# Optimization experiments

Measured on AMD Instinct MI355X. Metric: run time of the kernel, lower is better.

Reference implementation:

```python
import jax, jax.numpy as jnp
import numpy as np

B, N, D = 32, 64, 256

def _gelu(x):
    return jax.nn.gelu(x, approximate=False)

def setup_inputs() -> dict:
    key = jax.random.key(0)
    ks = jax.random.split(key, 16)
    def w(k, shape):
        fan_in = shape[0]
        return (jax.random.normal(k, shape, jnp.float32) / np.float32(np.sqrt(fan_in)))
    return {
        "dataset_embedding": jax.random.normal(ks[0], (B, D), jnp.float32),
        "variable_embeddings": jax.random.normal(ks[1], (B, N, D), jnp.float32),
        "claim_context": jax.random.normal(ks[2], (B, D), jnp.float32),
        "dge_w1": w(ks[3], (2 * D, D)), "dge_b1": jnp.zeros((D,), jnp.float32),
        "dge_w2": w(ks[4], (D, D)),     "dge_b2": jnp.zeros((D,), jnp.float32),
        "cge_w1": w(ks[5], (2 * D, D)), "cge_b1": jnp.zeros((D,), jnp.float32),
        "cge_w2": w(ks[6], (D, D)),     "cge_b2": jnp.zeros((D,), jnp.float32),
        "dep_w1": w(ks[7], (4 * D, D)), "dep_b1": jnp.zeros((D,), jnp.float32),
        "dep_w2": w(ks[8], (D, 1)),     "dep_b2": jnp.zeros((1,), jnp.float32),
        "cep_w1": w(ks[9], (4 * D, D)), "cep_b1": jnp.zeros((D,), jnp.float32),
        "cep_w2": w(ks[10], (D, 1)),    "cep_b2": jnp.zeros((1,), jnp.float32),
        "gate_w1": w(ks[11], (3, 64)),  "gate_b1": jnp.zeros((64,), jnp.float32),
        "gate_w2": w(ks[12], (64, 1)),  "gate_b2": jnp.zeros((1,), jnp.float32),
        "n_samples": 500,
    }

def _encode(ve, ctx, w1, b1, w2, b2):
    # Sequential(Linear(2d,d), GELU, Linear(d,d), GELU); dropout=0 (eval)
    x = jnp.concatenate([ve, jnp.broadcast_to(ctx[:, None, :], ve.shape)], axis=-1)
    h = _gelu(x @ w1 + b1)
    return _gelu(h @ w2 + b2)

def _predict_edges(ve_enc, ctx, w1, b1, w2, b2):
    # var_with_context: [B,N,2D]; edge features cat([var_i, var_j]) @ w1
    # == (vwc @ w1[:2D]) broadcast over i + (vwc @ w1[2D:]) broadcast over j
    vwc = jnp.concatenate([ve_enc, jnp.broadcast_to(ctx[:, None, :], ve_enc.shape)], axis=-1)
    wi, wj = w1[: 2 * D], w1[2 * D :]
    fi = vwc @ wi  # [B,N,D]
    fj = vwc @ wj  # [B,N,D]
    h = _gelu(fi[:, :, None, :] + fj[:, None, :, :] + b1)  # [B,N,N,D]
    logits = jnp.einsum("bijd,do->bij", h, w2) + b2[0]
    eye = jnp.eye(N, dtype=bool)
    return jnp.where(eye[None, :, :], jnp.float32(-1e9), logits)

def reference(dataset_embedding, variable_embeddings, claim_context,
              dge_w1, dge_b1, dge_w2, dge_b2,
              cge_w1, cge_b1, cge_w2, cge_b2,
              dep_w1, dep_b1, dep_w2, dep_b2,
              cep_w1, cep_b1, cep_w2, cep_b2,
              gate_w1, gate_b1, gate_w2, gate_b2,
              n_samples):
    avg_claim_confidence = 0.5
    var_data = _encode(variable_embeddings, dataset_embedding, dge_w1, dge_b1, dge_w2, dge_b2)
    var_claim = _encode(variable_embeddings, claim_context, cge_w1, cge_b1, cge_w2, cge_b2)
    W_data_logits = _predict_edges(var_data, dataset_embedding, dep_w1, dep_b1, dep_w2, dep_b2)
    W_claim_logits = _predict_edges(var_claim, claim_context, cep_w1, cep_b1, cep_w2, cep_b2)

    p = jax.nn.sigmoid(W_data_logits)
    eps = jnp.float32(1e-8)
    data_entropy = -(p * jnp.log(p + eps) + (1 - p) * jnp.log(1 - p + eps)).mean(axis=(1, 2))  # [B]

    ns = jnp.full((B,), min(n_samples / 1000.0, 1.0), jnp.float32)
    cc = jnp.full((B,), avg_claim_confidence, jnp.float32)
    gf = jnp.stack([ns, cc, data_entropy], axis=-1)  # [B,3]
    gate = jax.nn.sigmoid(_gelu(gf @ gate_w1 + gate_b1) @ gate_w2 + gate_b2)  # [B,1]
    gate = gate[:, :, None]  # [B,1,1]

    W_post_logits = gate * W_data_logits + (1 - gate) * W_claim_logits

    # NOTEARS: h(W) = tr(expm(W o W)) - n, W = sigmoid(logits)
    Wsig = jax.nn.sigmoid(W_post_logits)
    M = jax.vmap(jax.scipy.linalg.expm)(Wsig * Wsig)
    acyc = (jnp.trace(M, axis1=1, axis2=2) - N).mean()

    W_posterior = jax.nn.sigmoid(W_post_logits)
    return (W_posterior, acyc)
```

## Files before the change

### kernel.cpp

```cpp
#include <hip/hip_runtime.h>
#include <hip/hip_bf16.h>


#define LDS_STRIDE 260
#define ES 68

__device__ __forceinline__ float gelu_f(float x) {
    float z = fabsf(x) * 0.70710678118654752440f;
    float t = __builtin_amdgcn_rcpf(fmaf(0.3275911f, z, 1.0f));
    float p = t * fmaf(t, fmaf(t, fmaf(t, fmaf(t, 1.061405429f, -1.453152027f),
                                       1.421413741f), -0.284496736f), 0.254829592f);
    float e = __expf(-z * z);
    float erfv = fmaf(-p, e, 1.0f);
    erfv = copysignf(erfv, x);
    return 0.5f * x * (1.0f + erfv);
}
__device__ __forceinline__ float sigmoid_f(float x) {
    return 1.0f / (1.0f + expf(-x));
}
__device__ __forceinline__ float f4c(const float4& v, int k) {
    return k == 0 ? v.x : k == 1 ? v.y : k == 2 ? v.z : v.w;
}
__device__ __forceinline__ float4 ld4(const float* __restrict__ buf, int r, int c) {
    return *(const float4*)&buf[r * ES + c];
}

__global__ __launch_bounds__(256) void k0_ctx(
    const float* __restrict__ ds, const float* __restrict__ cc,
    const float* __restrict__ dge_w1, const float* __restrict__ dge_b1,
    const float* __restrict__ cge_w1, const float* __restrict__ cge_b1,
    const float* __restrict__ dep_w1, const float* __restrict__ dep_b1,
    const float* __restrict__ cep_w1, const float* __restrict__ cep_b1,
    float* __restrict__ ctxproj)
{
    const int b = blockIdx.x;
    const int which = blockIdx.y;
    const float* ctx; const float* W; const float* bias;
    switch (which) {
        case 0:  ctx = ds; W = dge_w1 + 256 * 256; bias = dge_b1; break;
        case 1:  ctx = cc; W = cge_w1 + 256 * 256; bias = cge_b1; break;
        case 2:  ctx = ds; W = dep_w1 + 256 * 256; bias = dep_b1; break;
        case 3:  ctx = ds; W = dep_w1 + 768 * 256; bias = nullptr; break;
        case 4:  ctx = cc; W = cep_w1 + 256 * 256; bias = cep_b1; break;
        default: ctx = cc; W = cep_w1 + 768 * 256; bias = nullptr; break;
    }
    __shared__ float sctx[256];
    const int tid = threadIdx.x;
    sctx[tid] = ctx[b * 256 + tid];
    __syncthreads();
    float acc = 0.0f;
    #pragma unroll 2
    for (int k = 0; k < 256; k += 4) {
        float4 c4 = *(const float4*)&sctx[k];
        acc = fmaf(c4.x, W[(k + 0) * 256 + tid], acc);
        acc = fmaf(c4.y, W[(k + 1) * 256 + tid], acc);
        acc = fmaf(c4.z, W[(k + 2) * 256 + tid], acc);
        acc = fmaf(c4.w, W[(k + 3) * 256 + tid], acc);
    }
    if (bias) acc += bias[tid];
    ctxproj[(which * 32 + b) * 256 + tid] = acc;
}

__device__ __forceinline__ void gemm_ks(const float* __restrict__ src,
                                        const float* __restrict__ W,
                                        int ks0, int t0, float acc[8][4])
{
    #pragma unroll
    for (int r = 0; r < 8; ++r)
        #pragma unroll
        for (int c = 0; c < 4; ++c) acc[r][c] = 0.0f;
    #pragma unroll 2
    for (int k = ks0; k < ks0 + 32; k += 4) {
        float4 wv0 = *(const float4*)&W[(k + 0) * 256 + t0];
        float4 wv1 = *(const float4*)&W[(k + 1) * 256 + t0];
        float4 wv2 = *(const float4*)&W[(k + 2) * 256 + t0];
        float4 wv3 = *(const float4*)&W[(k + 3) * 256 + t0];
        float4 a[8];
        #pragma unroll
        for (int r = 0; r < 8; ++r) a[r] = *(const float4*)&src[r * LDS_STRIDE + k];
        float4 wvs[4] = {wv0, wv1, wv2, wv3};
        #pragma unroll
        for (int kk = 0; kk < 4; ++kk) {
            float4 wv = wvs[kk];
            #pragma unroll
            for (int r = 0; r < 8; ++r) {
                float av = f4c(a[r], kk);
                acc[r][0] = fmaf(av, wv.x, acc[r][0]);
                acc[r][1] = fmaf(av, wv.y, acc[r][1]);
                acc[r][2] = fmaf(av, wv.z, acc[r][2]);
                acc[r][3] = fmaf(av, wv.w, acc[r][3]);
            }
        }
    }
}

__device__ __forceinline__ void write_part(float* __restrict__ part, int w, int t0,
                                           const float acc[8][4])
{
    #pragma unroll
    for (int r = 0; r < 8; ++r) {
        float4 o = {acc[r][0], acc[r][1], acc[r][2], acc[r][3]};
        *(float4*)&part[(w * 8 + r) * 256 + t0] = o;
    }
}

__device__ __forceinline__ float4 reduce_part(const float* __restrict__ part, int r, int t0)
{
    float4 s = {0.0f, 0.0f, 0.0f, 0.0f};
    #pragma unroll
    for (int w = 0; w < 8; ++w) {
        float4 v = *(const float4*)&part[(w * 8 + r) * 256 + t0];
        s.x += v.x; s.y += v.y; s.z += v.z; s.w += v.w;
    }
    return s;
}

__global__ __launch_bounds__(512) void k1_encode(
    const float* __restrict__ ve_g,
    const float* __restrict__ dge_w1, const float* __restrict__ dge_w2, const float* __restrict__ dge_b2,
    const float* __restrict__ cge_w1, const float* __restrict__ cge_w2, const float* __restrict__ cge_b2,
    const float* __restrict__ dep_w1, const float* __restrict__ cep_w1,
    const float* __restrict__ ctxproj,
    float* __restrict__ fi_dep, float* __restrict__ fjt_dep,
    float* __restrict__ fi_cep, float* __restrict__ fjt_cep)
{
    __shared__ float sve[8 * LDS_STRIDE];
    __shared__ float sA[8 * LDS_STRIDE];
    __shared__ float sB[8 * LDS_STRIDE];
    __shared__ float part[8 * 8 * 256];

    const int tid = threadIdx.x;
    const int b = blockIdx.x >> 3;
    const int chunk = blockIdx.x & 7;
    const int n0 = chunk * 8;

    const int w  = tid >> 6;
    const int t0 = (tid & 63) * 4;
    const int ks0 = w * 32;

    {
        int idx = tid * 4;
        int r = idx >> 8, k = idx & 255;
        *(float4*)&sve[r * LDS_STRIDE + k] = *(const float4*)&ve_g[(b * 64 + n0) * 256 + idx];
    }
    __syncthreads();

    float acc[8][4];

    gemm_ks(sve, dge_w1, ks0, t0, acc);
    write_part(part, w, t0, acc);
    __syncthreads();
    {
        float4 s = reduce_part(part, w, t0);
        float4 cp = *(const float4*)&ctxproj[(0 * 32 + b) * 256 + t0];
        float4 o = {gelu_f(s.x + cp.x), gelu_f(s.y + cp.y), gelu_f(s.z + cp.z), gelu_f(s.w + cp.w)};
        *(float4*)&sA[w * LDS_STRIDE + t0] = o;
    }
    __syncthreads();

    gemm_ks(sA, dge_w2, ks0, t0, acc);
    write_part(part, w, t0, acc);
    __syncthreads();
    {
        float4 s = reduce_part(part, w, t0);
        float4 bv = *(const float4*)&dge_b2[t0];
        float4 o = {gelu_f(s.x + bv.x), gelu_f(s.y + bv.y), gelu_f(s.z + bv.z), gelu_f(s.w + bv.w)};
        *(float4*)&sB[w * LDS_STRIDE + t0] = o;
    }
    __syncthreads();

    gemm_ks(sB, dep_w1, ks0, t0, acc);
    write_part(part, w, t0, acc);
    __syncthreads();
    {
        float4 s = reduce_part(part, w, t0);
        float4 cp = *(const float4*)&ctxproj[(2 * 32 + b) * 256 + t0];
        float4 o = {s.x + cp.x, s.y + cp.y, s.z + cp.z, s.w + cp.w};
        *(float4*)&fi_dep[(b * 64 + n0 + w) * 256 + t0] = o;
    }
    __syncthreads();

    gemm_ks(sB, dep_w1 + 512 * 256, ks0, t0, acc);
    write_part(part, w, t0, acc);
    __syncthreads();
    {
        float4 s = reduce_part(part, w, t0);
        float4 cp = *(const float4*)&ctxproj[(3 * 32 + b) * 256 + t0];
        float4 o = {s.x + cp.x, s.y + cp.y, s.z + cp.z, s.w + cp.w};
        *(float4*)&sA[w * LDS_STRIDE + t0] = o;
    }
    __syncthreads();
    {
        int t = tid & 255, half = tid >> 8;
        float v0 = sA[(half * 4 + 0) * LDS_STRIDE + t];
        float v1 = sA[(half * 4 + 1) * LDS_STRIDE + t];
        float v2 = sA[(half * 4 + 2) * LDS_STRIDE + t];
        float v3 = sA[(half * 4 + 3) * LDS_STRIDE + t];
        float4 o = {v0, v1, v2, v3};
        *(float4*)&fjt_dep[(b * 256 + t) * 64 + n0 + half * 4] = o;
    }

    gemm_ks(sve, cge_w1, ks0, t0, acc);
    write_part(part, w, t0, acc);
    __syncthreads();
    {
        float4 s = reduce_part(part, w, t0);
        float4 cp = *(const float4*)&ctxproj[(1 * 32 + b) * 256 + t0];
        float4 o = {gelu_f(s.x + cp.x), gelu_f(s.y + cp.y), gelu_f(s.z + cp.z), gelu_f(s.w + cp.w)};
        *(float4*)&sB[w * LDS_STRIDE + t0] = o;
    }
    __syncthreads();

    gemm_ks(sB, cge_w2, ks0, t0, acc);
    write_part(part, w, t0, acc);
    __syncthreads();
    {
        float4 s = reduce_part(part, w, t0);
        float4 bv = *(const float4*)&cge_b2[t0];
        float4 o = {gelu_f(s.x + bv.x), gelu_f(s.y + bv.y), gelu_f(s.z + bv.z), gelu_f(s.w + bv.w)};
        *(float4*)&sA[w * LDS_STRIDE + t0] = o;
    }
    __syncthreads();

    gemm_ks(sA, cep_w1, ks0, t0, acc);
    write_part(part, w, t0, acc);
    __syncthreads();
    {
        float4 s = reduce_part(part, w, t0);
        float4 cp = *(const float4*)&ctxproj[(4 * 32 + b) * 256 + t0];
        float4 o = {s.x + cp.x, s.y + cp.y, s.z + cp.z, s.w + cp.w};
        *(float4*)&fi_cep[(b * 64 + n0 + w) * 256 + t0] = o;
    }
    __syncthreads();

    gemm_ks(sA, cep_w1 + 512 * 256, ks0, t0, acc);
    write_part(part, w, t0, acc);
    __syncthreads();
    {
        float4 s = reduce_part(part, w, t0);
        float4 cp = *(const float4*)&ctxproj[(5 * 32 + b) * 256 + t0];
        float4 o = {s.x + cp.x, s.y + cp.y, s.z + cp.z, s.w + cp.w};
        *(float4*)&sB[w * LDS_STRIDE + t0] = o;
    }
    __syncthreads();
    {
        int t = tid & 255, half = tid >> 8;
        float v0 = sB[(half * 4 + 0) * LDS_STRIDE + t];
        float v1 = sB[(half * 4 + 1) * LDS_STRIDE + t];
        float v2 = sB[(half * 4 + 2) * LDS_STRIDE + t];
        float v3 = sB[(half * 4 + 3) * LDS_STRIDE + t];
        float4 o = {v0, v1, v2, v3};
        *(float4*)&fjt_cep[(b * 256 + t) * 64 + n0 + half * 4] = o;
    }
}

__global__ __launch_bounds__(512) void k3_edges(
    const float* __restrict__ fi_dep, const float* __restrict__ fjt_dep,
    const float* __restrict__ fi_cep, const float* __restrict__ fjt_cep,
    const float* __restrict__ dep_w2, const float* __restrict__ dep_b2,
    const float* __restrict__ cep_w2, const float* __restrict__ cep_b2,
    float* __restrict__ Wd, float* __restrict__ Wc, float* __restrict__ entp)
{
    __shared__ float fjD_s[64 * 64];
    __shared__ float fjC_s[64 * 64];
    __shared__ float fiD_s[4][256];
    __shared__ float fiC_s[4][256];
    __shared__ float w2D_s[256];
    __shared__ float w2C_s[256];
    __shared__ float redD[8][64];
    __shared__ float redC[8][64];

    const int b   = blockIdx.x >> 4;
    const int ig  = blockIdx.x & 15;
    const int tid = threadIdx.x;
    const int s   = tid >> 6;
    const int j   = tid & 63;
    const int row = s & 3;
    const int dh  = s >> 2;

    if (tid < 256) {
        int rr = tid >> 6, c = (tid & 63) * 4;
        *(float4*)&fiD_s[rr][c] = *(const float4*)&fi_dep[(b * 64 + ig * 4 + rr) * 256 + c];
    } else {
        int t2 = tid - 256;
        int rr = t2 >> 6, c = (t2 & 63) * 4;
        *(float4*)&fiC_s[rr][c] = *(const float4*)&fi_cep[(b * 64 + ig * 4 + rr) * 256 + c];
    }
    if (tid < 64) {
        *(float4*)&w2D_s[tid * 4] = *(const float4*)&dep_w2[tid * 4];
    } else if (tid < 128) {
        int t = tid - 64;
        *(float4*)&w2C_s[t * 4] = *(const float4*)&cep_w2[t * 4];
    }

    float accD = 0.0f, accC = 0.0f;

    for (int c0 = 0; c0 < 256; c0 += 64) {
        if (c0) __syncthreads();
        {
            const float4* sD = (const float4*)(fjt_dep + (b * 256 + c0) * 64);
            const float4* sC = (const float4*)(fjt_cep + (b * 256 + c0) * 64);
            ((float4*)fjD_s)[tid]       = sD[tid];
            ((float4*)fjD_s)[tid + 512] = sD[tid + 512];
            ((float4*)fjC_s)[tid]       = sC[tid];
            ((float4*)fjC_s)[tid + 512] = sC[tid + 512];
        }
        __syncthreads();

        const int d0 = dh * 32;
        #pragma unroll 4
        for (int d = d0; d < d0 + 32; d += 2) {
            float fid0 = fiD_s[row][c0 + d];
            float fid1 = fiD_s[row][c0 + d + 1];
            float fic0 = fiC_s[row][c0 + d];
            float fic1 = fiC_s[row][c0 + d + 1];
            float fjd0 = fjD_s[(d + 0) * 64 + j];
            float fjd1 = fjD_s[(d + 1) * 64 + j];
            float fjc0 = fjC_s[(d + 0) * 64 + j];
            float fjc1 = fjC_s[(d + 1) * 64 + j];
            float wd0 = w2D_s[c0 + d], wd1 = w2D_s[c0 + d + 1];
            float wc0 = w2C_s[c0 + d], wc1 = w2C_s[c0 + d + 1];
            accD = fmaf(gelu_f(fid0 + fjd0), wd0, accD);
            accD = fmaf(gelu_f(fid1 + fjd1), wd1, accD);
            accC = fmaf(gelu_f(fic0 + fjc0), wc0, accC);
            accC = fmaf(gelu_f(fic1 + fjc1), wc1, accC);
        }
    }

    redD[s][j] = accD;
    redC[s][j] = accC;
    __syncthreads();

    if (s < 4) {
        const int i = ig * 4 + s;
        float lD = (redD[s][j] + redD[s + 4][j]) + dep_b2[0];
        float lC = (redC[s][j] + redC[s + 4][j]) + cep_b2[0];
        if (j == i) { lD = -1e9f; lC = -1e9f; }
        Wd[(b * 64 + i) * 64 + j] = lD;
        Wc[(b * 64 + i) * 64 + j] = lC;

        float p = sigmoid_f(lD);
        float e = -(p * logf(p + 1e-8f) + (1.0f - p) * logf(1.0f - p + 1e-8f));
        #pragma unroll
        for (int off = 32; off; off >>= 1) e += __shfl_down(e, off);
        if (j == 0) entp[b * 64 + i] = e;
    }
}

__device__ __forceinline__ void mm64f(const float* __restrict__ A, const float* __restrict__ B,
                                      int r0, int c0, float acc[4][4])
{
    #pragma unroll
    for (int i = 0; i < 4; ++i)
        #pragma unroll
        for (int j = 0; j < 4; ++j) acc[i][j] = 0.0f;
    for (int kb = 0; kb < 64; kb += 4) {
        float4 xa[4];
        #pragma unroll
        for (int i = 0; i < 4; ++i) xa[i] = ld4(A, r0 + i, kb);
        #pragma unroll
        for (int kk = 0; kk < 4; ++kk) {
            float4 rv = ld4(B, kb + kk, c0);
            float rj[4] = {rv.x, rv.y, rv.z, rv.w};
            #pragma unroll
            for (int i = 0; i < 4; ++i) {
                float xv = f4c(xa[i], kk);
                #pragma unroll
                for (int j = 0; j < 4; ++j) acc[i][j] = fmaf(xv, rj[j], acc[i][j]);
            }
        }
    }
}

__device__ __forceinline__ void mm64d(const float* __restrict__ A, const float* __restrict__ B,
                                      int r0, int c0, double acc[4][4])
{
    #pragma unroll
    for (int i = 0; i < 4; ++i)
        #pragma unroll
        for (int j = 0; j < 4; ++j) acc[i][j] = 0.0;
    for (int kb = 0; kb < 64; kb += 4) {
        float4 xa[4];
        #pragma unroll
        for (int i = 0; i < 4; ++i) xa[i] = ld4(A, r0 + i, kb);
        #pragma unroll
        for (int kk = 0; kk < 4; ++kk) {
            float4 rv = ld4(B, kb + kk, c0);
            double rj[4] = {(double)rv.x, (double)rv.y, (double)rv.z, (double)rv.w};
            #pragma unroll
            for (int i = 0; i < 4; ++i) {
                double xv = (double)f4c(xa[i], kk);
                #pragma unroll
                for (int j = 0; j < 4; ++j) acc[i][j] = fma(xv, rj[j], acc[i][j]);
            }
        }
    }
}

__global__ __launch_bounds__(256) void k6_gate_expm(
    const float* __restrict__ Wd, const float* __restrict__ Wc,
    const float* __restrict__ entp,
    const float* __restrict__ gw1, const float* __restrict__ gb1,
    const float* __restrict__ gw2, const float* __restrict__ gb2,
    const int* __restrict__ n_samples,
    float* __restrict__ out, float* __restrict__ traces)
{
    __shared__ float Xs [64 * ES];
    __shared__ float X2s[64 * ES];
    __shared__ float X3s[64 * ES];
    __shared__ float Ra [64 * ES];
    __shared__ float Rb [64 * ES];
    __shared__ float sgate;
    __shared__ float sent;
    __shared__ int ssexp;

    const int b = blockIdx.x;
    const int tid = threadIdx.x;

    const float C2 = 0.5f, C3 = 1.0f/6.0f, C4 = 1.0f/24.0f, C5 = 1.0f/120.0f;
    const float C6 = 1.0f/720.0f, C7 = 1.0f/5040.0f, C8 = 1.0f/40320.0f;
    const float C9 = 1.0f/362880.0f, C10 = 1.0f/3628800.0f, C11 = 1.0f/39916800.0f;
    const float C12 = 1.0f/479001600.0f, C13 = 1.0f/6227020800.0f;

    if (tid == 0) {
        float s = 0.0f;
        for (int c = 0; c < 64; ++c) s += entp[b * 64 + c];
        sent = s / 4096.0f;
    }
    __syncthreads();
    if (tid < 64) {
        float ns = fminf((float)n_samples[0] / 1000.0f, 1.0f);
        float ccf = 0.5f;
        float pre = ns * gw1[tid] + ccf * gw1[64 + tid] + sent * gw1[128 + tid] + gb1[tid];
        float hid = gelu_f(pre) * gw2[tid];
        #pragma unroll
        for (int off = 32; off; off >>= 1) hid += __shfl_down(hid, off);
        if (tid == 0) sgate = sigmoid_f(hid + gb2[0]);
    }
    __syncthreads();
    const float g = sgate;

    for (int idx = tid; idx < 4096; idx += 256) {
        float d = Wd[b * 4096 + idx];
        float c = Wc[b * 4096 + idx];
        float post = g * d + (1.0f - g) * c;
        float sg = sigmoid_f(post);
        out[b * 4096 + idx] = sg;
        Xs[(idx >> 6) * ES + (idx & 63)] = sg * sg;
    }
    __syncthreads();

    if (tid < 64) {
        float cs = 0.0f;
        for (int r = 0; r < 64; ++r) cs += Xs[r * ES + tid];
        #pragma unroll
        for (int off = 32; off; off >>= 1) cs = fmaxf(cs, __shfl_down(cs, off));
        if (tid == 0) {
            int se = 0;
            if (cs > 1.0f) se = (int)ceilf(log2f(cs));
            if (se < 0) se = 0;
            if (se > 12) se = 12;
            ssexp = se;
        }
    }
    __syncthreads();
    const int sexp = ssexp;
    const float scale = ldexpf(1.0f, -sexp);
    for (int idx = tid; idx < 4096; idx += 256) {
        Xs[(idx >> 6) * ES + (idx & 63)] *= scale;
    }
    __syncthreads();

    const int rq = tid >> 4, cq = tid & 15;
    const int r0 = rq * 4, c0 = cq * 4;
    float acc[4][4];

    mm64f(Xs, Xs, r0, c0, acc);
    #pragma unroll
    for (int i = 0; i < 4; ++i) {
        float4 o = {acc[i][0], acc[i][1], acc[i][2], acc[i][3]};
        *(float4*)&X2s[(r0 + i) * ES + c0] = o;
    }
    __syncthreads();

    mm64f(X2s, Xs, r0, c0, acc);
    #pragma unroll
    for (int i = 0; i < 4; ++i) {
        float4 o = {acc[i][0], acc[i][1], acc[i][2], acc[i][3]};
        *(float4*)&X3s[(r0 + i) * ES + c0] = o;
    }
    __syncthreads();

    mm64f(Xs, X3s, r0, c0, acc);
    #pragma unroll
    for (int i = 0; i < 4; ++i) {
        float4 xv = ld4(Xs, r0 + i, c0);
        float4 x2 = ld4(X2s, r0 + i, c0);
        float4 x3 = ld4(X3s, r0 + i, c0);
        float o[4];
        #pragma unroll
        for (int j = 0; j < 4; ++j) {
            o[j] = C13 * acc[i][j] + C12 * f4c(x3, j) + C10 * f4c(xv, j) + C11 * f4c(x2, j)
                 + ((r0 + i) == (c0 + j) ? C9 : 0.0f);
        }
        float4 ov = {o[0], o[1], o[2], o[3]};
        *(float4*)&Ra[(r0 + i) * ES + c0] = ov;
    }
    __syncthreads();

    mm64f(Ra, X3s, r0, c0, acc);
    #pragma unroll
    for (int i = 0; i < 4; ++i) {
        float4 xv = ld4(Xs, r0 + i, c0);
        float4 x2 = ld4(X2s, r0 + i, c0);
        float o[4];
        #pragma unroll
        for (int j = 0; j < 4; ++j) {
            o[j] = acc[i][j] + C7 * f4c(xv, j) + C8 * f4c(x2, j)
                 + ((r0 + i) == (c0 + j) ? C6 : 0.0f);
        }
        float4 ov = {o[0], o[1], o[2], o[3]};
        *(float4*)&Rb[(r0 + i) * ES + c0] = ov;
    }
    __syncthreads();

    mm64f(Rb, X3s, r0, c0, acc);
    #pragma unroll
    for (int i = 0; i < 4; ++i) {
        float4 xv = ld4(Xs, r0 + i, c0);
        float4 x2 = ld4(X2s, r0 + i, c0);
        float o[4];
        #pragma unroll
        for (int j = 0; j < 4; ++j) {
            o[j] = acc[i][j] + C4 * f4c(xv, j) + C5 * f4c(x2, j)
                 + ((r0 + i) == (c0 + j) ? C3 : 0.0f);
        }
        float4 ov = {o[0], o[1], o[2], o[3]};
        *(float4*)&Ra[(r0 + i) * ES + c0] = ov;
    }
    __syncthreads();

    mm64f(Ra, X3s, r0, c0, acc);
    #pragma unroll
    for (int i = 0; i < 4; ++i) {
        float4 xv = ld4(Xs, r0 + i, c0);
        float4 x2 = ld4(X2s, r0 + i, c0);
        float o[4];
        #pragma unroll
        for (int j = 0; j < 4; ++j) {
            o[j] = acc[i][j] + f4c(xv, j) + C2 * f4c(x2, j)
                 + ((r0 + i) == (c0 + j) ? 1.0f : 0.0f);
        }
        float4 ov = {o[0], o[1], o[2], o[3]};
        *(float4*)&Rb[(r0 + i) * ES + c0] = ov;
    }
    __syncthreads();

    float* cur = Rb;
    float* oth = Ra;
    for (int sq = 0; sq < sexp; ++sq) {
        double dacc[4][4];
        mm64d(cur, cur, r0, c0, dacc);
        #pragma unroll
        for (int i = 0; i < 4; ++i) {
            float4 o = {(float)dacc[i][0], (float)dacc[i][1], (float)dacc[i][2], (float)dacc[i][3]};
            *(float4*)&oth[(r0 + i) * ES + c0] = o;
        }
        __syncthreads();
        float* t = cur; cur = oth; oth = t;
    }

    if (tid == 0) {
        double tr = 0.0;
        for (int i = 0; i < 64; ++i) tr += (double)cur[i * ES + i];
        traces[b] = (float)tr;
    }
}

__global__ void k7_acyc(const float* __restrict__ traces, float* __restrict__ out)
{
    if (threadIdx.x == 0 && blockIdx.x == 0) {
        double s = 0.0;
        for (int b = 0; b < 32; ++b) s += (double)traces[b];
        out[131072] = (float)(s / 32.0 - 64.0);
    }
}

extern "C" void kernel_launch(void* const* d_in, const int* in_sizes, int n_in,
                              void* d_out, int out_size, void* d_ws, size_t ws_size,
                              hipStream_t stream)
{
    (void)in_sizes; (void)n_in; (void)out_size; (void)ws_size;

    const float* ds     = (const float*)d_in[0];
    const float* ve     = (const float*)d_in[1];
    const float* cc     = (const float*)d_in[2];
    const float* dge_w1 = (const float*)d_in[3];
    const float* dge_b1 = (const float*)d_in[4];
    const float* dge_w2 = (const float*)d_in[5];
    const float* dge_b2 = (const float*)d_in[6];
    const float* cge_w1 = (const float*)d_in[7];
    const float* cge_b1 = (const float*)d_in[8];
    const float* cge_w2 = (const float*)d_in[9];
    const float* cge_b2 = (const float*)d_in[10];
    const float* dep_w1 = (const float*)d_in[11];
    const float* dep_b1 = (const float*)d_in[12];
    const float* dep_w2 = (const float*)d_in[13];
    const float* dep_b2 = (const float*)d_in[14];
    const float* cep_w1 = (const float*)d_in[15];
    const float* cep_b1 = (const float*)d_in[16];
    const float* cep_w2 = (const float*)d_in[17];
    const float* cep_b2 = (const float*)d_in[18];
    const float* gw1    = (const float*)d_in[19];
    const float* gb1    = (const float*)d_in[20];
    const float* gw2    = (const float*)d_in[21];
    const float* gb2    = (const float*)d_in[22];
    const int*   nsamp  = (const int*)d_in[23];

    float* ws = (float*)d_ws;
    float* ctxproj = ws;
    float* fi_dep  = ctxproj + 49152;
    float* fjt_dep = fi_dep + 524288;
    float* fi_cep  = fjt_dep + 524288;
    float* fjt_cep = fi_cep + 524288;
    float* Wd      = fjt_cep + 524288;
    float* Wc      = Wd + 131072;
    float* entp    = Wc + 131072;
    float* traces  = entp + 2048;

    float* outp = (float*)d_out;

    k0_ctx<<<dim3(32, 6), 256, 0, stream>>>(ds, cc, dge_w1, dge_b1, cge_w1, cge_b1,
                                            dep_w1, dep_b1, cep_w1, cep_b1, ctxproj);
    k1_encode<<<256, 512, 0, stream>>>(ve, dge_w1, dge_w2, dge_b2,
                                       cge_w1, cge_w2, cge_b2,
                                       dep_w1, cep_w1, ctxproj,
                                       fi_dep, fjt_dep, fi_cep, fjt_cep);
    k3_edges<<<512, 512, 0, stream>>>(fi_dep, fjt_dep, fi_cep, fjt_cep,
                                      dep_w2, dep_b2, cep_w2, cep_b2,
                                      Wd, Wc, entp);
    k6_gate_expm<<<32, 256, 0, stream>>>(Wd, Wc, entp, gw1, gb1, gw2, gb2,
                                         nsamp, outp, traces);
    k7_acyc<<<1, 64, 0, stream>>>(traces, outp);
}
```

Measured before the change: 129.5 us.

## Split encoder chains across blocks, halve partial buffer, widen expm kernel

The encoder kernel now runs the data and claim chains in separate blocks (512 blocks instead of 256), which doubles parallelism. The per-block split-K partial buffer is halved by having the upper warps add their partials in place, and context projections are loaded once up front. The expm kernel goes from 256 to 512 threads with 2x4 output tiles, and its scalar loops for the entropy sum and trace become wave shuffle reductions. The scaling threshold also changes so one fewer squaring step is used, which may shift accuracy a little in exchange for less work.

```diff
diff --git a/kernel.cpp b/kernel.cpp
--- a/kernel.cpp
+++ b/kernel.cpp
@@ -94,28 +94,40 @@
     }
 }
 
-__device__ __forceinline__ void write_part(float* __restrict__ part, int w, int t0,
-                                           const float acc[8][4])
-{
-    #pragma unroll
-    for (int r = 0; r < 8; ++r) {
-        float4 o = {acc[r][0], acc[r][1], acc[r][2], acc[r][3]};
-        *(float4*)&part[(w * 8 + r) * 256 + t0] = o;
-    }
-}
-
-__device__ __forceinline__ float4 reduce_part(const float* __restrict__ part, int r, int t0)
+__device__ __forceinline__ void part_write_rmw(float* __restrict__ part, int w, int t0,
+                                               const float acc[8][4])
+{
+    if (w < 4) {
+        #pragma unroll
+        for (int r = 0; r < 8; ++r) {
+            float4 o = {acc[r][0], acc[r][1], acc[r][2], acc[r][3]};
+            *(float4*)&part[(w * 8 + r) * 256 + t0] = o;
+        }
+    }
+    __syncthreads();
+    if (w >= 4) {
+        #pragma unroll
+        for (int r = 0; r < 8; ++r) {
+            float4 v = *(const float4*)&part[((w - 4) * 8 + r) * 256 + t0];
+            float4 o = {v.x + acc[r][0], v.y + acc[r][1], v.z + acc[r][2], v.w + acc[r][3]};
+            *(float4*)&part[((w - 4) * 8 + r) * 256 + t0] = o;
+        }
+    }
+    __syncthreads();
+}
+
+__device__ __forceinline__ float4 reduce4(const float* __restrict__ part, int r, int t0)
 {
     float4 s = {0.0f, 0.0f, 0.0f, 0.0f};
     #pragma unroll
-    for (int w = 0; w < 8; ++w) {
-        float4 v = *(const float4*)&part[(w * 8 + r) * 256 + t0];
+    for (int sl = 0; sl < 4; ++sl) {
+        float4 v = *(const float4*)&part[(sl * 8 + r) * 256 + t0];
         s.x += v.x; s.y += v.y; s.z += v.z; s.w += v.w;
     }
     return s;
 }
 
-__global__ __launch_bounds__(512) void k1_encode(
+__global__ __launch_bounds__(512, 4) void k1_encode(
     const float* __restrict__ ve_g,
     const float* __restrict__ dge_w1, const float* __restrict__ dge_w2, const float* __restrict__ dge_b2,
     const float* __restrict__ cge_w1, const float* __restrict__ cge_w2, const float* __restrict__ cge_b2,
@@ -127,16 +139,33 @@
     __shared__ float sve[8 * LDS_STRIDE];
     __shared__ float sA[8 * LDS_STRIDE];
     __shared__ float sB[8 * LDS_STRIDE];
-    __shared__ float part[8 * 8 * 256];
-
-    const int tid = threadIdx.x;
-    const int b = blockIdx.x >> 3;
-    const int chunk = blockIdx.x & 7;
-    const int n0 = chunk * 8;
+    __shared__ float part[4 * 8 * 256];
+
+    const int tid   = threadIdx.x;
+    const int blk   = blockIdx.x;
+    const int chain = blk & 1;
+    const int chunk = (blk >> 1) & 7;
+    const int b     = blk >> 4;
+    const int n0    = chunk * 8;
+
+    const float* w1   = chain ? cge_w1 : dge_w1;
+    const float* w2   = chain ? cge_w2 : dge_w2;
+    const float* b2   = chain ? cge_b2 : dge_b2;
+    const float* epw  = chain ? cep_w1 : dep_w1;
+    float* fi  = chain ? fi_cep  : fi_dep;
+    float* fjt = chain ? fjt_cep : fjt_dep;
+    const int cp_s1 = chain ? 1 : 0;
+    const int cp_fi = chain ? 4 : 2;
+    const int cp_fj = chain ? 5 : 3;
 
     const int w  = tid >> 6;
     const int t0 = (tid & 63) * 4;
     const int ks0 = w * 32;
+
+    float4 cp1 = *(const float4*)&ctxproj[(cp_s1 * 32 + b) * 256 + t0];
+    float4 bv2 = *(const float4*)&b2[t0];
+    float4 cpf = *(const float4*)&ctxproj[(cp_fi * 32 + b) * 256 + t0];
+    float4 cpj = *(const float4*)&ctxproj[(cp_fj * 32 + b) * 256 + t0];
 
     {
         int idx = tid * 4;
@@ -147,46 +176,40 @@
 
     float acc[8][4];
 
-    gemm_ks(sve, dge_w1, ks0, t0, acc);
-    write_part(part, w, t0, acc);
-    __syncthreads();
+    gemm_ks(sve, w1, ks0, t0, acc);
+    part_write_rmw(part, w, t0, acc);
     {
-        float4 s = reduce_part(part, w, t0);
-        float4 cp = *(const float4*)&ctxproj[(0 * 32 + b) * 256 + t0];
-        float4 o = {gelu_f(s.x + cp.x), gelu_f(s.y + cp.y), gelu_f(s.z + cp.z), gelu_f(s.w + cp.w)};
+        float4 s = reduce4(part, w, t0);
+        float4 o = {gelu_f(s.x + cp1.x), gelu_f(s.y + cp1.y),
+                    gelu_f(s.z + cp1.z), gelu_f(s.w + cp1.w)};
         *(float4*)&sA[w * LDS_STRIDE + t0] = o;
     }
     __syncthreads();
 
-    gemm_ks(sA, dge_w2, ks0, t0, acc);
-    write_part(part, w, t0, acc);
-    __syncthreads();
+    gemm_ks(sA, w2, ks0, t0, acc);
+    part_write_rmw(part, w, t0, acc);
     {
-        float4 s = reduce_part(part, w, t0);
-        float4 bv = *(const float4*)&dge_b2[t0];
-        float4 o = {gelu_f(s.x + bv.x), gelu_f(s.y + bv.y), gelu_f(s.z + bv.z), gelu_f(s.w + bv.w)};
+        float4 s = reduce4(part, w, t0);
+        float4 o = {gelu_f(s.x + bv2.x), gelu_f(s.y + bv2.y),
+                    gelu_f(s.z + bv2.z), gelu_f(s.w + bv2.w)};
         *(float4*)&sB[w * LDS_STRIDE + t0] = o;
     }
     __syncthreads();
 
-    gemm_ks(sB, dep_w1, ks0, t0, acc);
-    write_part(part, w, t0, acc);
-    __syncthreads();
+    gemm_ks(sB, epw, ks0, t0, acc);
+    part_write_rmw(part, w, t0, acc);
     {
-        float4 s = reduce_part(part, w, t0);
-        float4 cp = *(const float4*)&ctxproj[(2 * 32 + b) * 256 + t0];
-        float4 o = {s.x + cp.x, s.y + cp.y, s.z + cp.z, s.w + cp.w};
-        *(float4*)&fi_dep[(b * 64 + n0 + w) * 256 + t0] = o;
-    }
-    __syncthreads();
-
-    gemm_ks(sB, dep_w1 + 512 * 256, ks0, t0, acc);
-    write_part(part, w, t0, acc);
-    __syncthreads();
+        float4 s = reduce4(part, w, t0);
+        float4 o = {s.x + cpf.x, s.y + cpf.y, s.z + cpf.z, s.w + cpf.w};
+        *(float4*)&fi[(b * 64 + n0 + w) * 256 + t0] = o;
+    }
+    __syncthreads();
+
+    gemm_ks(sB, epw + 512 * 256, ks0, t0, acc);
+    part_write_rmw(part, w, t0, acc);
     {
-        float4 s = reduce_part(part, w, t0);
-        float4 cp = *(const float4*)&ctxproj[(3 * 32 + b) * 256 + t0];
-        float4 o = {s.x + cp.x, s.y + cp.y, s.z + cp.z, s.w + cp.w};
+        float4 s = reduce4(part, w, t0);
+        float4 o = {s.x + cpj.x, s.y + cpj.y, s.z + cpj.z, s.w + cpj.w};
         *(float4*)&sA[w * LDS_STRIDE + t0] = o;
     }
     __syncthreads();
@@ -197,60 +220,7 @@
         float v2 = sA[(half * 4 + 2) * LDS_STRIDE + t];
         float v3 = sA[(half * 4 + 3) * LDS_STRIDE + t];
         float4 o = {v0, v1, v2, v3};
-        *(float4*)&fjt_dep[(b * 256 + t) * 64 + n0 + half * 4] = o;
-    }
-
-    gemm_ks(sve, cge_w1, ks0, t0, acc);
-    write_part(part, w, t0, acc);
-    __syncthreads();
-    {
-        float4 s = reduce_part(part, w, t0);
-        float4 cp = *(const float4*)&ctxproj[(1 * 32 + b) * 256 + t0];
-        float4 o = {gelu_f(s.x + cp.x), gelu_f(s.y + cp.y), gelu_f(s.z + cp.z), gelu_f(s.w + cp.w)};
-        *(float4*)&sB[w * LDS_STRIDE + t0] = o;
-    }
-    __syncthreads();
-
-    gemm_ks(sB, cge_w2, ks0, t0, acc);
-    write_part(part, w, t0, acc);
-    __syncthreads();
-    {
-        float4 s = reduce_part(part, w, t0);
-        float4 bv = *(const float4*)&cge_b2[t0];
-        float4 o = {gelu_f(s.x + bv.x), gelu_f(s.y + bv.y), gelu_f(s.z + bv.z), gelu_f(s.w + bv.w)};
-        *(float4*)&sA[w * LDS_STRIDE + t0] = o;
-    }
-    __syncthreads();
-
-    gemm_ks(sA, cep_w1, ks0, t0, acc);
-    write_part(part, w, t0, acc);
-    __syncthreads();
-    {
-        float4 s = reduce_part(part, w, t0);
-        float4 cp = *(const float4*)&ctxproj[(4 * 32 + b) * 256 + t0];
-        float4 o = {s.x + cp.x, s.y + cp.y, s.z + cp.z, s.w + cp.w};
-        *(float4*)&fi_cep[(b * 64 + n0 + w) * 256 + t0] = o;
-    }
-    __syncthreads();
-
-    gemm_ks(sA, cep_w1 + 512 * 256, ks0, t0, acc);
-    write_part(part, w, t0, acc);
-    __syncthreads();
-    {
-        float4 s = reduce_part(part, w, t0);
-        float4 cp = *(const float4*)&ctxproj[(5 * 32 + b) * 256 + t0];
-        float4 o = {s.x + cp.x, s.y + cp.y, s.z + cp.z, s.w + cp.w};
-        *(float4*)&sB[w * LDS_STRIDE + t0] = o;
-    }
-    __syncthreads();
-    {
-        int t = tid & 255, half = tid >> 8;
-        float v0 = sB[(half * 4 + 0) * LDS_STRIDE + t];
-        float v1 = sB[(half * 4 + 1) * LDS_STRIDE + t];
-        float v2 = sB[(half * 4 + 2) * LDS_STRIDE + t];
-        float v3 = sB[(half * 4 + 3) * LDS_STRIDE + t];
-        float4 o = {v0, v1, v2, v3};
-        *(float4*)&fjt_cep[(b * 256 + t) * 64 + n0 + half * 4] = o;
+        *(float4*)&fjt[(b * 256 + t) * 64 + n0 + half * 4] = o;
     }
 }
 
@@ -347,57 +317,57 @@
     }
 }
 
-__device__ __forceinline__ void mm64f(const float* __restrict__ A, const float* __restrict__ B,
-                                      int r0, int c0, float acc[4][4])
-{
-    #pragma unroll
-    for (int i = 0; i < 4; ++i)
+__device__ __forceinline__ void mm64f2(const float* __restrict__ A, const float* __restrict__ B,
+                                       int r0, int c0, float acc[2][4])
+{
+    #pragma unroll
+    for (int i = 0; i < 2; ++i)
         #pragma unroll
         for (int j = 0; j < 4; ++j) acc[i][j] = 0.0f;
     for (int kb = 0; kb < 64; kb += 4) {
-        float4 xa[4];
-        #pragma unroll
-        for (int i = 0; i < 4; ++i) xa[i] = ld4(A, r0 + i, kb);
+        float4 a0 = ld4(A, r0 + 0, kb);
+        float4 a1 = ld4(A, r0 + 1, kb);
         #pragma unroll
         for (int kk = 0; kk < 4; ++kk) {
             float4 rv = ld4(B, kb + kk, c0);
-            float rj[4] = {rv.x, rv.y, rv.z, rv.w};
-            #pragma unroll
-            for (int i = 0; i < 4; ++i) {
-                float xv = f4c(xa[i], kk);
-                #pragma unroll
-                for (int j = 0; j < 4; ++j) acc[i][j] = fmaf(xv, rj[j], acc[i][j]);
-            }
-        }
-    }
-}
-
-__device__ __forceinline__ void mm64d(const float* __restrict__ A, const float* __restrict__ B,
-                                      int r0, int c0, double acc[4][4])
-{
-    #pragma unroll
-    for (int i = 0; i < 4; ++i)
+            float x0 = f4c(a0, kk), x1 = f4c(a1, kk);
+            acc[0][0] = fmaf(x0, rv.x, acc[0][0]);
+            acc[0][1] = fmaf(x0, rv.y, acc[0][1]);
+            acc[0][2] = fmaf(x0, rv.z, acc[0][2]);
+            acc[0][3] = fmaf(x0, rv.w, acc[0][3]);
+            acc[1][0] = fmaf(x1, rv.x, acc[1][0]);
+            acc[1][1] = fmaf(x1, rv.y, acc[1][1]);
+            acc[1][2] = fmaf(x1, rv.z, acc[1][2]);
+            acc[1][3] = fmaf(x1, rv.w, acc[1][3]);
+        }
+    }
+}
+
+__device__ __forceinline__ void mm64d2(const float* __restrict__ A, const float* __restrict__ B,
+                                       int r0, int c0, double acc[2][4])
+{
+    #pragma unroll
+    for (int i = 0; i < 2; ++i)
         #pragma unroll
         for (int j = 0; j < 4; ++j) acc[i][j] = 0.0;
     for (int kb = 0; kb < 64; kb += 4) {
-        float4 xa[4];
-        #pragma unroll
-        for (int i = 0; i < 4; ++i) xa[i] = ld4(A, r0 + i, kb);
+        float4 a0 = ld4(A, r0 + 0, kb);
+        float4 a1 = ld4(A, r0 + 1, kb);
         #pragma unroll
         for (int kk = 0; kk < 4; ++kk) {
             float4 rv = ld4(B, kb + kk, c0);
             double rj[4] = {(double)rv.x, (double)rv.y, (double)rv.z, (double)rv.w};
+            double x0 = (double)f4c(a0, kk), x1 = (double)f4c(a1, kk);
             #pragma unroll
-            for (int i = 0; i < 4; ++i) {
-                double xv = (double)f4c(xa[i], kk);
-                #pragma unroll
-                for (int j = 0; j < 4; ++j) acc[i][j] = fma(xv, rj[j], acc[i][j]);
+            for (int j = 0; j < 4; ++j) {
+                acc[0][j] = fma(x0, rj[j], acc[0][j]);
+                acc[1][j] = fma(x1, rj[j], acc[1][j]);
             }
         }
     }
 }
 
-__global__ __launch_bounds__(256) void k6_gate_expm(
+__global__ __launch_bounds__(512) void k6_gate_expm(
     const float* __restrict__ Wd, const float* __restrict__ Wc,
     const float* __restrict__ entp,
     const float* __restrict__ gw1, const float* __restrict__ gb1,
@@ -422,10 +392,11 @@
     const float C9 = 1.0f/362880.0f, C10 = 1.0f/3628800.0f, C11 = 1.0f/39916800.0f;
     const float C12 = 1.0f/479001600.0f, C13 = 1.0f/6227020800.0f;
 
-    if (tid == 0) {
-        float s = 0.0f;
-        for (int c = 0; c < 64; ++c) s += entp[b * 64 + c];
-        sent = s / 4096.0f;
+    if (tid < 64) {
+        float v = entp[b * 64 + tid];
+        #pragma unroll
+        for (int off = 32; off; off >>= 1) v += __shfl_down(v, off);
+        if (tid == 0) sent = v / 4096.0f;
     }
     __syncthreads();
     if (tid < 64) {
@@ -440,7 +411,7 @@
     __syncthreads();
     const float g = sgate;
 
-    for (int idx = tid; idx < 4096; idx += 256) {
+    for (int idx = tid; idx < 4096; idx += 512) {
         float d = Wd[b * 4096 + idx];
         float c = Wc[b * 4096 + idx];
         float post = g * d + (1.0f - g) * c;
@@ -457,7 +428,7 @@
         for (int off = 32; off; off >>= 1) cs = fmaxf(cs, __shfl_down(cs, off));
         if (tid == 0) {
             int se = 0;
-            if (cs > 1.0f) se = (int)ceilf(log2f(cs));
+            if (cs > 2.0f) se = (int)ceilf(log2f(cs * 0.5f));
             if (se < 0) se = 0;
             if (se > 12) se = 12;
             ssexp = se;
@@ -466,34 +437,34 @@
     __syncthreads();
     const int sexp = ssexp;
     const float scale = ldexpf(1.0f, -sexp);
-    for (int idx = tid; idx < 4096; idx += 256) {
+    for (int idx = tid; idx < 4096; idx += 512) {
         Xs[(idx >> 6) * ES + (idx & 63)] *= scale;
     }
     __syncthreads();
 
-    const int rq = tid >> 4, cq = tid & 15;
-    const int r0 = rq * 4, c0 = cq * 4;
-    float acc[4][4];
-
-    mm64f(Xs, Xs, r0, c0, acc);
-    #pragma unroll
-    for (int i = 0; i < 4; ++i) {
+    const int r0 = (tid >> 4) * 2;
+    const int c0 = (tid & 15) * 4;
+    float acc[2][4];
+
+    mm64f2(Xs, Xs, r0, c0, acc);
+    #pragma unroll
+    for (int i = 0; i < 2; ++i) {
         float4 o = {acc[i][0], acc[i][1], acc[i][2], acc[i][3]};
         *(float4*)&X2s[(r0 + i) * ES + c0] = o;
     }
     __syncthreads();
 
-    mm64f(X2s, Xs, r0, c0, acc);
-    #pragma unroll
-    for (int i = 0; i < 4; ++i) {
+    mm64f2(X2s, Xs, r0, c0, acc);
+    #pragma unroll
+    for (int i = 0; i < 2; ++i) {
         float4 o = {acc[i][0], acc[i][1], acc[i][2], acc[i][3]};
         *(float4*)&X3s[(r0 + i) * ES + c0] = o;
     }
     __syncthreads();
 
-    mm64f(Xs, X3s, r0, c0, acc);
-    #pragma unroll
-    for (int i = 0; i < 4; ++i) {
+    mm64f2(Xs, X3s, r0, c0, acc);
+    #pragma unroll
+    for (int i = 0; i < 2; ++i) {
         float4 xv = ld4(Xs, r0 + i, c0);
         float4 x2 = ld4(X2s, r0 + i, c0);
         float4 x3 = ld4(X3s, r0 + i, c0);
@@ -508,9 +479,9 @@
     }
     __syncthreads();
 
-    mm64f(Ra, X3s, r0, c0, acc);
-    #pragma unroll
-    for (int i = 0; i < 4; ++i) {
+    mm64f2(Ra, X3s, r0, c0, acc);
+    #pragma unroll
+    for (int i = 0; i < 2; ++i) {
         float4 xv = ld4(Xs, r0 + i, c0);
         float4 x2 = ld4(X2s, r0 + i, c0);
         float o[4];
@@ -524,9 +495,9 @@
     }
     __syncthreads();
 
-    mm64f(Rb, X3s, r0, c0, acc);
-    #pragma unroll
-    for (int i = 0; i < 4; ++i) {
+    mm64f2(Rb, X3s, r0, c0, acc);
+    #pragma unroll
+    for (int i = 0; i < 2; ++i) {
         float4 xv = ld4(Xs, r0 + i, c0);
         float4 x2 = ld4(X2s, r0 + i, c0);
         float o[4];
@@ -540,9 +511,9 @@
     }
     __syncthreads();
 
-    mm64f(Ra, X3s, r0, c0, acc);
-    #pragma unroll
-    for (int i = 0; i < 4; ++i) {
+    mm64f2(Ra, X3s, r0, c0, acc);
+    #pragma unroll
+    for (int i = 0; i < 2; ++i) {
         float4 xv = ld4(Xs, r0 + i, c0);
         float4 x2 = ld4(X2s, r0 + i, c0);
         float o[4];
@@ -559,10 +530,10 @@
     float* cur = Rb;
     float* oth = Ra;
     for (int sq = 0; sq < sexp; ++sq) {
-        double dacc[4][4];
-        mm64d(cur, cur, r0, c0, dacc);
-        #pragma unroll
-        for (int i = 0; i < 4; ++i) {
+        double dacc[2][4];
+        mm64d2(cur, cur, r0, c0, dacc);
+        #pragma unroll
+        for (int i = 0; i < 2; ++i) {
             float4 o = {(float)dacc[i][0], (float)dacc[i][1], (float)dacc[i][2], (float)dacc[i][3]};
             *(float4*)&oth[(r0 + i) * ES + c0] = o;
         }
@@ -570,10 +541,11 @@
         float* t = cur; cur = oth; oth = t;
     }
 
-    if (tid == 0) {
-        double tr = 0.0;
-        for (int i = 0; i < 64; ++i) tr += (double)cur[i * ES + i];
-        traces[b] = (float)tr;
+    if (tid < 64) {
+        double v = (double)cur[tid * ES + tid];
+        #pragma unroll
+        for (int off = 32; off; off >>= 1) v += __shfl_down(v, off);
+        if (tid == 0) traces[b] = (float)v;
     }
 }
 
@@ -632,14 +604,14 @@
 
     k0_ctx<<<dim3(32, 6), 256, 0, stream>>>(ds, cc, dge_w1, dge_b1, cge_w1, cge_b1,
                                             dep_w1, dep_b1, cep_w1, cep_b1, ctxproj);
-    k1_encode<<<256, 512, 0, stream>>>(ve, dge_w1, dge_w2, dge_b2,
+    k1_encode<<<512, 512, 0, stream>>>(ve, dge_w1, dge_w2, dge_b2,
                                        cge_w1, cge_w2, cge_b2,
                                        dep_w1, cep_w1, ctxproj,
                                        fi_dep, fjt_dep, fi_cep, fjt_cep);
     k3_edges<<<512, 512, 0, stream>>>(fi_dep, fjt_dep, fi_cep, fjt_cep,
                                       dep_w2, dep_b2, cep_w2, cep_b2,
                                       Wd, Wc, entp);
-    k6_gate_expm<<<32, 256, 0, stream>>>(Wd, Wc, entp, gw1, gb1, gw2, gb2,
+    k6_gate_expm<<<32, 512, 0, stream>>>(Wd, Wc, entp, gw1, gb1, gw2, gb2,
                                          nsamp, outp, traces);
     k7_acyc<<<1, 64, 0, stream>>>(traces, outp);
 }
```

Result: faster. 122.8 us (-5.1%).
